# Performance work log

Measured on AMD Instinct MI355X. Metric: run time of the kernel, lower is better.

## Reference

```python
import jax, jax.numpy as jnp
import numpy as np
from jax import lax

B, EMB, CIN, COUT, K, H, W = 16, 768, 64, 64, 3, 112, 112
HID = EMB // 4  # reduction_ratio=4
TOTAL = COUT * CIN * K * K


def setup_inputs() -> dict:
    key = jax.random.key(0)
    k1, k2, k3, k4 = jax.random.split(key, 4)
    cls_token = jax.random.normal(k1, (B, 1, EMB), dtype=jnp.float32)
    features = jax.random.normal(k2, (B, CIN, H, W), dtype=jnp.float32)
    W1 = jax.random.normal(k3, (EMB, HID), dtype=jnp.float32) * 0.02
    b1 = jnp.zeros((HID,), dtype=jnp.float32)
    W2 = jax.random.normal(k4, (HID, TOTAL), dtype=jnp.float32) * 0.01
    b2 = jnp.zeros((TOTAL,), dtype=jnp.float32)
    return {"cls_token": cls_token, "features": features,
            "W1": W1, "b1": b1, "W2": W2, "b2": b2}


def _per_sample_conv(feat, kern):
    # feat: (CIN, H, W); kern: (COUT, CIN, K, K) -> (COUT, H, W)
    out = lax.conv_general_dilated(
        feat[None], kern, window_strides=(1, 1), padding="SAME",
        dimension_numbers=("NCHW", "OIHW", "NCHW"))
    return out[0]


def reference(cls_token, features, W1, b1, W2, b2):
    # Dynamic kernel generation from CLS token
    x = cls_token[:, 0, :]                      # (B, EMB)
    h = jax.nn.relu(x @ W1 + b1)                # (B, HID)
    params = jnp.tanh(h @ W2 + b2)              # (B, TOTAL)
    kernel = params.reshape(B, COUT, CIN, K, K)
    # Per-sample convolution (equivalent to unfold + bmm in torch)
    conv_feat = jax.vmap(_per_sample_conv)(features, kernel)  # (B, COUT, H, W)
    # in_channels == out_channels -> identity shortcut
    return conv_feat + features
```

## Files before the change

### kernel.cpp

```cpp
#include <hip/hip_runtime.h>
#include <hip/hip_bf16.h>

#define BB   16
#define EMB  768
#define CIN  64
#define COUT 64
#define HH   112
#define WW   112
#define HID  192
#define TOTAL 36864
#define KSZ  576
#define SCOLS 114
#define CELL  128
#define ROWB (SCOLS * CELL)

typedef short bf16x8 __attribute__((ext_vector_type(8)));
typedef float f32x4  __attribute__((ext_vector_type(4)));
typedef int   i32x4  __attribute__((ext_vector_type(4)));

static __device__ __forceinline__ unsigned short f2bf(float f) {
    unsigned u = __float_as_uint(f);
    u += 0x7FFF + ((u >> 16) & 1);
    return (unsigned short)(u >> 16);
}

static __device__ __forceinline__ bf16x8 pack8(const float* v) {
    bf16x8 r;
    #pragma unroll
    for (int j = 0; j < 8; ++j) r[j] = (short)f2bf(v[j]);
    return r;
}

__global__ __launch_bounds__(256) void mlp1_kernel(const float* __restrict__ cls,
                                                   const float* __restrict__ W1,
                                                   const float* __restrict__ b1,
                                                   float* __restrict__ h) {
    __shared__ float xs[EMB];
    __shared__ float red[16][17];
    const int b   = blockIdx.x / 12;
    const int jg  = blockIdx.x - 12 * b;
    const int tid = threadIdx.x;
    for (int i = tid; i < EMB; i += 256) xs[i] = cls[b * EMB + i];
    __syncthreads();
    const int j16 = tid & 15;
    const int kq  = tid >> 4;
    const int j   = jg * 16 + j16;
    float acc = 0.f;
    #pragma unroll
    for (int k = kq * 48; k < kq * 48 + 48; ++k) acc += xs[k] * W1[k * HID + j];
    red[j16][kq] = acc;
    __syncthreads();
    if (tid < 16) {
        float s = b1[jg * 16 + tid];
        #pragma unroll
        for (int q = 0; q < 16; ++q) s += red[tid][q];
        h[b * HID + jg * 16 + tid] = fmaxf(s, 0.f);
    }
}

__global__ __launch_bounds__(256) void mlp2_kernel(const float* __restrict__ h,
                                                   const float* __restrict__ W2,
                                                   const float* __restrict__ b2,
                                                   unsigned short* __restrict__ Ag) {
    __shared__ float hs[16 * 193];
    const int tid = threadIdx.x;
    for (int i = tid; i < BB * HID; i += 256) {
        const int bb = i / HID;
        hs[bb * 193 + (i - bb * HID)] = h[i];
    }
    __syncthreads();
    const int wave = tid >> 6;
    const int lane = tid & 63;
    const int lg   = lane >> 4;
    const int ln   = lane & 15;
    const int t0   = (blockIdx.x * 4 + wave) * 16;

    bf16x8 a6[6];
    #pragma unroll
    for (int kk = 0; kk < 6; ++kk) {
        float v[8];
        #pragma unroll
        for (int j = 0; j < 8; ++j) v[j] = hs[ln * 193 + kk * 32 + lg * 8 + j];
        a6[kk] = pack8(v);
    }

    f32x4 acc = (f32x4){0.f, 0.f, 0.f, 0.f};
    #pragma unroll
    for (int kk = 0; kk < 6; ++kk) {
        float w[8];
        #pragma unroll
        for (int j = 0; j < 8; ++j)
            w[j] = W2[(size_t)(kk * 32 + lg * 8 + j) * TOTAL + t0 + ln];
        acc = __builtin_amdgcn_mfma_f32_16x16x32_bf16(a6[kk], pack8(w), acc, 0, 0, 0);
    }

    const int t    = t0 + ln;
    const float bias = b2[t];
    const int co  = t / KSZ;
    const int rem = t - co * KSZ;
    const int ci  = rem / 9;
    const int p9  = rem - ci * 9;
    const float idv = (p9 == 4 && co == ci) ? 1.f : 0.f;
    unsigned short* pA = Ag + (size_t)(p9 * 64 + co) * 64 + ci;
    #pragma unroll
    for (int rg = 0; rg < 4; ++rg) {
        const int bi = lg * 4 + rg;
        pA[(size_t)bi * TOTAL] = f2bf(tanhf(acc[rg] + bias) + idv);
    }
}

__global__ __launch_bounds__(256) void conv_kernel(const float* __restrict__ feat,
                                                   const unsigned short* __restrict__ Ag,
                                                   float* __restrict__ out) {
    __shared__ __align__(16) char lds[4 * ROWB];
    const int tid = threadIdx.x;
    const int bid  = (blockIdx.x & 7) * 112 + (blockIdx.x >> 3);
    const int b    = bid / 56;
    const int tile = bid - b * 56;
    const int y0   = tile * 2;

    if (tid < 64) {
        const int zr = tid >> 4, zc = ((tid >> 3) & 1) ? (SCOLS - 1) : 0, zs = tid & 7;
        *(i32x4*)(lds + (zr * SCOLS + zc) * CELL + zs * 16) = (i32x4){0, 0, 0, 0};
    }

    {
        const int o  = tid >> 5;
        const int rr = (tid >> 3) & 3;
        const int xs = tid & 7;
        if (xs < 7) {
            const int y  = y0 - 1 + rr;
            const bool yv = (unsigned)y < HH;
            const float* fp = feat + (((size_t)b * CIN + o * 8) * HH + y) * WW + 4 * xs;
            const f32x4 z4 = {0.f, 0.f, 0.f, 0.f};
            char* ldsr = lds + rr * ROWB;
            #pragma unroll
            for (int sh = 0; sh < 2; ++sh) {
                f32x4 v[8][2];
                #pragma unroll
                for (int ss = 0; ss < 2; ++ss) {
                    const int s = sh * 2 + ss;
                    #pragma unroll
                    for (int j = 0; j < 8; ++j)
                        v[j][ss] = yv ? *(const f32x4*)(fp + (size_t)j * (HH * WW) + s * 28)
                                      : z4;
                }
                #pragma unroll
                for (int ss = 0; ss < 2; ++ss) {
                    const int s = sh * 2 + ss;
                    #pragma unroll
                    for (int j2 = 0; j2 < 4; ++j2) {
                        const int cell = 4 * (s * 7 + xs) + j2 + 1;
                        const int sl   = (o ^ (cell & 7) ^ rr) & 7;
                        const unsigned d0 = (unsigned)f2bf(v[0][ss][j2]) | ((unsigned)f2bf(v[1][ss][j2]) << 16);
                        const unsigned d1 = (unsigned)f2bf(v[2][ss][j2]) | ((unsigned)f2bf(v[3][ss][j2]) << 16);
                        const unsigned d2 = (unsigned)f2bf(v[4][ss][j2]) | ((unsigned)f2bf(v[5][ss][j2]) << 16);
                        const unsigned d3 = (unsigned)f2bf(v[6][ss][j2]) | ((unsigned)f2bf(v[7][ss][j2]) << 16);
                        *(i32x4*)(ldsr + cell * CELL + sl * 16) =
                            (i32x4){(int)d0, (int)d1, (int)d2, (int)d3};
                    }
                }
            }
        }
    }

    const int wave = tid >> 6;
    const int lane = tid & 63;
    const int cog  = wave & 1;
    const int r    = wave >> 1;
    const int lg   = lane >> 4;
    const int ln   = lane & 15;
    const unsigned short* Ab = Ag + (size_t)b * 9 * 4096;
    bf16x8 af[9][2][2];
    #pragma unroll
    for (int p9 = 0; p9 < 9; ++p9)
        #pragma unroll
        for (int ct = 0; ct < 2; ++ct)
            #pragma unroll
            for (int cib = 0; cib < 2; ++cib)
                af[p9][ct][cib] = *(const bf16x8*)(Ab + (size_t)(p9 * 64 + cog * 32 + ct * 16 + ln) * 64
                                                   + cib * 32 + lg * 8);
    __syncthreads();

    f32x4 acc[2][7];
    #pragma unroll
    for (int ct = 0; ct < 2; ++ct)
        #pragma unroll
        for (int t = 0; t < 7; ++t) acc[ct][t] = (f32x4){0.f, 0.f, 0.f, 0.f};

    #pragma unroll
    for (int p9 = 0; p9 < 9; ++p9) {
        const int kh = p9 / 3, kw = p9 - 3 * kh;
        const int rs = r + kh;
        const char* lbase = lds + rs * ROWB + (ln + kw) * CELL;
        const int   c7    = (ln + kw) & 7;
        #pragma unroll
        for (int cib = 0; cib < 2; ++cib) {
            const int sw = (((cib * 4 + lg) ^ c7 ^ rs) & 7) << 4;
            #pragma unroll
            for (int t = 0; t < 7; ++t) {
                const bf16x8 bf = *(const bf16x8*)(lbase + t * 2048 + sw);
                acc[0][t] = __builtin_amdgcn_mfma_f32_16x16x32_bf16(af[p9][0][cib], bf, acc[0][t], 0, 0, 0);
                acc[1][t] = __builtin_amdgcn_mfma_f32_16x16x32_bf16(af[p9][1][cib], bf, acc[1][t], 0, 0, 0);
            }
        }
    }

    const int y = y0 + r;
    float* ob = out + (((size_t)b * COUT + cog * 32 + lg * 4) * HH + y) * WW + ln;
    #pragma unroll
    for (int ct = 0; ct < 2; ++ct)
        #pragma unroll
        for (int t = 0; t < 7; ++t)
            #pragma unroll
            for (int rg = 0; rg < 4; ++rg)
                ob[((size_t)(ct * 16 + rg)) * HH * WW + t * 16] = acc[ct][t][rg];
}

extern "C" void kernel_launch(void* const* d_in, const int* in_sizes, int n_in,
                              void* d_out, int out_size, void* d_ws, size_t ws_size,
                              hipStream_t stream) {
    const float* cls      = (const float*)d_in[0];
    const float* features = (const float*)d_in[1];
    const float* W1       = (const float*)d_in[2];
    const float* b1       = (const float*)d_in[3];
    const float* W2       = (const float*)d_in[4];
    const float* b2       = (const float*)d_in[5];
    float* out = (float*)d_out;

    float*          h  = (float*)d_ws;
    unsigned short* Ag = (unsigned short*)(h + BB * HID);

    mlp1_kernel<<<192, 256, 0, stream>>>(cls, W1, b1, h);
    mlp2_kernel<<<TOTAL / 64, 256, 0, stream>>>(h, W2, b2, Ag);
    conv_kernel<<<56 * BB, 256, 0, stream>>>(feat\
ures, Ag, out);
}
```

Measured before the change: 58.32 us.

## Split conv input channels into two halves to halve LDS and weight registers

The conv kernel now stages input channels in two 32-channel halves, cutting the LDS tile from 4x114x128 to 4x114x64 bytes. Weight fragments are loaded per half and per tap inside the loop instead of being held in a large register array up front. Launch bounds now request 4 blocks per CU. The aim is higher occupancy through lower LDS and register use, at the cost of an extra barrier between halves and less overlap of the global loads with the MFMA work.

Measured after the change: 56.68 us. -2.8%, faster.

```diff
diff --git a/kernel.cpp b/kernel.cpp
--- a/kernel.cpp
+++ b/kernel.cpp
@@ -11,12 +11,13 @@
 #define TOTAL 36864
 #define KSZ  576
 #define SCOLS 114
-#define CELL  128
-#define ROWB (SCOLS * CELL)
+#define CELLH 64
+#define ROWBH (SCOLS * CELLH)
 
 typedef short bf16x8 __attribute__((ext_vector_type(8)));
 typedef float f32x4  __attribute__((ext_vector_type(4)));
 typedef int   i32x4  __attribute__((ext_vector_type(4)));
+typedef int   i32x2  __attribute__((ext_vector_type(2)));
 
 static __device__ __forceinline__ unsigned short f2bf(float f) {
     unsigned u = __float_as_uint(f);
@@ -109,60 +110,15 @@
     }
 }
 
-__global__ __launch_bounds__(256) void conv_kernel(const float* __restrict__ feat,
-                                                   const unsigned short* __restrict__ Ag,
-                                                   float* __restrict__ out) {
-    __shared__ __align__(16) char lds[4 * ROWB];
+__global__ __launch_bounds__(256, 4) void conv_kernel(const float* __restrict__ feat,
+                                                      const unsigned short* __restrict__ Ag,
+                                                      float* __restrict__ out) {
+    __shared__ __align__(16) char lds[4 * ROWBH];
     const int tid = threadIdx.x;
     const int bid  = (blockIdx.x & 7) * 112 + (blockIdx.x >> 3);
     const int b    = bid / 56;
     const int tile = bid - b * 56;
     const int y0   = tile * 2;
-
-    if (tid < 64) {
-        const int zr = tid >> 4, zc = ((tid >> 3) & 1) ? (SCOLS - 1) : 0, zs = tid & 7;
-        *(i32x4*)(lds + (zr * SCOLS + zc) * CELL + zs * 16) = (i32x4){0, 0, 0, 0};
-    }
-
-    {
-        const int o  = tid >> 5;
-        const int rr = (tid >> 3) & 3;
-        const int xs = tid & 7;
-        if (xs < 7) {
-            const int y  = y0 - 1 + rr;
-            const bool yv = (unsigned)y < HH;
-            const float* fp = feat + (((size_t)b * CIN + o * 8) * HH + y) * WW + 4 * xs;
-            const f32x4 z4 = {0.f, 0.f, 0.f, 0.f};
-            char* ldsr = lds + rr * ROWB;
-            #pragma unroll
-            for (int sh = 0; sh < 2; ++sh) {
-                f32x4 v[8][2];
-                #pragma unroll
-                for (int ss = 0; ss < 2; ++ss) {
-                    const int s = sh * 2 + ss;
-                    #pragma unroll
-                    for (int j = 0; j < 8; ++j)
-                        v[j][ss] = yv ? *(const f32x4*)(fp + (size_t)j * (HH * WW) + s * 28)
-                                      : z4;
-                }
-                #pragma unroll
-                for (int ss = 0; ss < 2; ++ss) {
-                    const int s = sh * 2 + ss;
-                    #pragma unroll
-                    for (int j2 = 0; j2 < 4; ++j2) {
-                        const int cell = 4 * (s * 7 + xs) + j2 + 1;
-                        const int sl   = (o ^ (cell & 7) ^ rr) & 7;
-                        const unsigned d0 = (unsigned)f2bf(v[0][ss][j2]) | ((unsigned)f2bf(v[1][ss][j2]) << 16);
-                        const unsigned d1 = (unsigned)f2bf(v[2][ss][j2]) | ((unsigned)f2bf(v[3][ss][j2]) << 16);
-                        const unsigned d2 = (unsigned)f2bf(v[4][ss][j2]) | ((unsigned)f2bf(v[5][ss][j2]) << 16);
-                        const unsigned d3 = (unsigned)f2bf(v[6][ss][j2]) | ((unsigned)f2bf(v[7][ss][j2]) << 16);
-                        *(i32x4*)(ldsr + cell * CELL + sl * 16) =
-                            (i32x4){(int)d0, (int)d1, (int)d2, (int)d3};
-                    }
-                }
-            }
-        }
-    }
 
     const int wave = tid >> 6;
     const int lane = tid & 63;
@@ -170,38 +126,72 @@
     const int r    = wave >> 1;
     const int lg   = lane >> 4;
     const int ln   = lane & 15;
+
+    const int so = tid >> 6;
+    const int sr = (tid >> 4) & 3;
+    const int sx = tid & 15;
+    const int sy = y0 - 1 + sr;
+    const bool sact = (sx < 14);
+    const bool syv  = sact && ((unsigned)sy < HH);
+    char* ldsr = lds + sr * ROWBH;
+    const f32x4 z4 = {0.f, 0.f, 0.f, 0.f};
+
+    f32x4 acc[2][7];
+    #pragma unroll
+    for (int ct = 0; ct < 2; ++ct)
+        #pragma unroll
+        for (int t = 0; t < 7; ++t) acc[ct][t] = (f32x4){0.f, 0.f, 0.f, 0.f};
+
     const unsigned short* Ab = Ag + (size_t)b * 9 * 4096;
-    bf16x8 af[9][2][2];
-    #pragma unroll
-    for (int p9 = 0; p9 < 9; ++p9)
-        #pragma unroll
-        for (int ct = 0; ct < 2; ++ct)
+
+    if (tid < 32) {
+        const int zr = tid >> 3, zc = ((tid >> 2) & 1) ? (SCOLS - 1) : 0, zs = tid & 3;
+        *(i32x4*)(lds + zr * ROWBH + zc * CELLH + zs * 16) = (i32x4){0, 0, 0, 0};
+    }
+
+    #pragma unroll
+    for (int h = 0; h < 2; ++h) {
+        if (h) __syncthreads();
+        if (sact) {
+            const float* fp = feat + (((size_t)b * CIN + h * 32 + so * 8) * HH + sy) * WW + 8 * sx;
             #pragma unroll
-            for (int cib = 0; cib < 2; ++cib)
-                af[p9][ct][cib] = *(const bf16x8*)(Ab + (size_t)(p9 * 64 + cog * 32 + ct * 16 + ln) * 64
-                                                   + cib * 32 + lg * 8);
-    __syncthreads();
-
-    f32x4 acc[2][7];
-    #pragma unroll
-    for (int ct = 0; ct < 2; ++ct)
-        #pragma unroll
-        for (int t = 0; t < 7; ++t) acc[ct][t] = (f32x4){0.f, 0.f, 0.f, 0.f};
-
-    #pragma unroll
-    for (int p9 = 0; p9 < 9; ++p9) {
-        const int kh = p9 / 3, kw = p9 - 3 * kh;
-        const int rs = r + kh;
-        const char* lbase = lds + rs * ROWB + (ln + kw) * CELL;
-        const int   c7    = (ln + kw) & 7;
-        #pragma unroll
-        for (int cib = 0; cib < 2; ++cib) {
-            const int sw = (((cib * 4 + lg) ^ c7 ^ rs) & 7) << 4;
+            for (int jb = 0; jb < 2; ++jb) {
+                f32x4 v[4][2];
+                #pragma unroll
+                for (int j = 0; j < 4; ++j)
+                    #pragma unroll
+                    for (int c = 0; c < 2; ++c)
+                        v[j][c] = syv ? *(const f32x4*)(fp + (size_t)(jb * 4 + j) * (HH * WW) + 4 * c)
+                                      : z4;
+                #pragma unroll
+                for (int i = 0; i < 8; ++i) {
+                    const int cell = 8 * sx + i + 1;
+                    const int sl   = (so ^ (cell & 3) ^ sr) & 3;
+                    const int c = i >> 2, e = i & 3;
+                    const unsigned d0 = (unsigned)f2bf(v[0][c][e]) | ((unsigned)f2bf(v[1][c][e]) << 16);
+                    const unsigned d1 = (unsigned)f2bf(v[2][c][e]) | ((unsigned)f2bf(v[3][c][e]) << 16);
+                    *(i32x2*)(ldsr + cell * CELLH + sl * 16 + jb * 8) = (i32x2){(int)d0, (int)d1};
+                }
+            }
+        }
+        __syncthreads();
+
+        #pragma unroll
+        for (int p9 = 0; p9 < 9; ++p9) {
+            const int kh = p9 / 3, kw = p9 - 3 * kh;
+            const int rs = r + kh;
+            const bf16x8 a0 = *(const bf16x8*)(Ab + (size_t)(p9 * 64 + cog * 32 + ln) * 64
+                                               + h * 32 + lg * 8);
+            const bf16x8 a1 = *(const bf16x8*)(Ab + (size_t)(p9 * 64 + cog * 32 + 16 + ln) * 64
+                                               + h * 32 + lg * 8);
+            const char* lbase = lds + rs * ROWBH;
             #pragma unroll
             for (int t = 0; t < 7; ++t) {
-                const bf16x8 bf = *(const bf16x8*)(lbase + t * 2048 + sw);
-                acc[0][t] = __builtin_amdgcn_mfma_f32_16x16x32_bf16(af[p9][0][cib], bf, acc[0][t], 0, 0, 0);
-                acc[1][t] = __builtin_amdgcn_mfma_f32_16x16x32_bf16(af[p9][1][cib], bf, acc[1][t], 0, 0, 0);
+                const int cell = ln + kw + 16 * t;
+                const int sl   = (lg ^ (cell & 3) ^ rs) & 3;
+                const bf16x8 bf = *(const bf16x8*)(lbase + cell * CELLH + sl * 16);
+                acc[0][t] = __builtin_amdgcn_mfma_f32_16x16x32_bf16(a0, bf, acc[0][t], 0, 0, 0);
+                acc[1][t] = __builtin_amdgcn_mfma_f32_16x16x32_bf16(a1, bf, acc[1][t], 0, 0, 0);
             }
         }
     }
@@ -233,6 +223,5 @@
 
     mlp1_kernel<<<192, 256, 0, stream>>>(cls, W1, b1, h);
     mlp2_kernel<<<TOTAL / 64, 256, 0, stream>>>(h, W2, b2, Ag);
-    conv_kernel<<<56 * BB, 256, 0, stream>>>(feat\
-ures, Ag, out);
-}
+    conv_kernel<<<56 * BB, 256, 0, stream>>>(features, Ag, out);
+}
```

## Pre-pack padded bf16 feature plane and stream into LDS via global_load_lds

Applied to the files above, without the earlier changes.

Adds a pre-pass, fused with the first MLP kernel, that converts features to a zero-padded channel-last bf16 buffer in workspace. The conv kernel then fills LDS directly with async global_load_lds copies that apply the XOR swizzle, replacing its per-block fp32 load, convert and LDS store. Each input row was previously converted once per overlapping tile, and the halo rows twice, so this removes redundant conversion and halves the bytes the conv kernel reads. The cost is an extra write and read of the bf16 buffer through global memory. It also relies on workspace being large enough for the padded plane.

Measured after the change: 60.58 us. 1.04x slower.

```diff
diff --git a/kernel.cpp b/kernel.cpp
--- a/kernel.cpp
+++ b/kernel.cpp
@@ -10,9 +10,9 @@
 #define HID  192
 #define TOTAL 36864
 #define KSZ  576
-#define SCOLS 114
-#define CELL  128
-#define ROWB (SCOLS * CELL)
+#define PW   114
+#define CELL 128
+#define ROWB (PW * CELL)
 
 typedef short bf16x8 __attribute__((ext_vector_type(8)));
 typedef float f32x4  __attribute__((ext_vector_type(4)));
@@ -31,30 +31,74 @@
     return r;
 }
 
-__global__ __launch_bounds__(256) void mlp1_kernel(const float* __restrict__ cls,
-                                                   const float* __restrict__ W1,
-                                                   const float* __restrict__ b1,
-                                                   float* __restrict__ h) {
-    __shared__ float xs[EMB];
-    __shared__ float red[16][17];
-    const int b   = blockIdx.x / 12;
-    const int jg  = blockIdx.x - 12 * b;
+#define GLOAD_LDS16(g, l) \
+    __builtin_amdgcn_global_load_lds((const __attribute__((address_space(1))) void*)(g), \
+                                     (__attribute__((address_space(3))) void*)(l), 16, 0, 0)
+
+__global__ __launch_bounds__(256) void pre_mlp1(const float* __restrict__ feat,
+                                                unsigned short* __restrict__ P,
+                                                const float* __restrict__ cls,
+                                                const float* __restrict__ W1,
+                                                const float* __restrict__ b1,
+                                                float* __restrict__ h) {
+    __shared__ float smem[EMB + 16 * 17];
+    const int bid = blockIdx.x;
     const int tid = threadIdx.x;
-    for (int i = tid; i < EMB; i += 256) xs[i] = cls[b * EMB + i];
-    __syncthreads();
-    const int j16 = tid & 15;
-    const int kq  = tid >> 4;
-    const int j   = jg * 16 + j16;
-    float acc = 0.f;
-    #pragma unroll
-    for (int k = kq * 48; k < kq * 48 + 48; ++k) acc += xs[k] * W1[k * HID + j];
-    red[j16][kq] = acc;
-    __syncthreads();
-    if (tid < 16) {
-        float s = b1[jg * 16 + tid];
-        #pragma unroll
-        for (int q = 0; q < 16; ++q) s += red[tid][q];
-        h[b * HID + jg * 16 + tid] = fmaxf(s, 0.f);
+
+    if (bid < HH * BB) {
+        const int b = bid & 15;
+        const int y = bid >> 4;
+        unsigned short* Prow = P + ((size_t)b * PW + y + 1) * (PW * 64);
+        if (tid < 16) {
+            const int cell = (tid >> 3) ? (PW - 1) : 0;
+            *(i32x4*)((char*)Prow + cell * CELL + (tid & 7) * 16) = (i32x4){0, 0, 0, 0};
+        }
+        const int o = tid >> 5;
+        const int q = tid & 31;
+        if (q < 28) {
+            const float* fb = feat + (((size_t)b * CIN + o * 8) * HH + y) * WW + 4 * q;
+            f32x4 v[8];
+            #pragma unroll
+            for (int j = 0; j < 8; ++j) v[j] = *(const f32x4*)(fb + (size_t)j * (HH * WW));
+            #pragma unroll
+            for (int i = 0; i < 4; ++i) {
+                unsigned short w[8];
+                #pragma unroll
+                for (int j = 0; j < 8; ++j) w[j] = f2bf(v[j][i]);
+                *(bf16x8*)(Prow + (size_t)(4 * q + i + 1) * 64 + o * 8) = *(bf16x8*)w;
+            }
+        }
+    } else if (bid < HH * BB + 32) {
+        const int idx = bid - HH * BB;
+        const int b = idx & 15;
+        unsigned short* Prow = P + ((size_t)b * PW + ((idx >> 4) ? (PW - 1) : 0)) * (PW * 64);
+        #pragma unroll
+        for (int k = 0; k < 4; ++k) {
+            const int i = tid + 256 * k;
+            if (i < 912) ((i32x4*)Prow)[i] = (i32x4){0, 0, 0, 0};
+        }
+    } else {
+        float* xs  = smem;
+        float* red = smem + EMB;
+        const int idx = bid - (HH * BB + 32);
+        const int b   = idx / 12;
+        const int jg  = idx - 12 * b;
+        for (int i = tid; i < EMB; i += 256) xs[i] = cls[b * EMB + i];
+        __syncthreads();
+        const int j16 = tid & 15;
+        const int kq  = tid >> 4;
+        const int j   = jg * 16 + j16;
+        float acc = 0.f;
+        #pragma unroll
+        for (int k = kq * 48; k < kq * 48 + 48; ++k) acc += xs[k] * W1[k * HID + j];
+        red[j16 * 17 + kq] = acc;
+        __syncthreads();
+        if (tid < 16) {
+            float s = b1[jg * 16 + tid];
+            #pragma unroll
+            for (int q = 0; q < 16; ++q) s += red[tid * 17 + q];
+            h[b * HID + jg * 16 + tid] = fmaxf(s, 0.f);
+        }
     }
 }
 
@@ -109,8 +153,8 @@
     }
 }
 
-__global__ __launch_bounds__(256) void conv_kernel(const float* __restrict__ feat,
-                                                   const unsigned short* __restrict__ Ag,
+__global__ __launch_bounds__(256) void conv_kernel(const unsigned short* __restrict__ Ag,
+                                                   const unsigned short* __restrict__ P,
                                                    float* __restrict__ out) {
     __shared__ __align__(16) char lds[4 * ROWB];
     const int tid = threadIdx.x;
@@ -119,49 +163,22 @@
     const int tile = bid - b * 56;
     const int y0   = tile * 2;
 
+    const char* Prow0 = (const char*)(P + ((size_t)b * PW + y0) * (PW * 64));
+    #pragma unroll
+    for (int it = 0; it < 14; ++it) {
+        const int i = it * 256 + tid;
+        const int s = i / 912;
+        const int j = i - s * 912;
+        const int c = j >> 3, g = j & 7;
+        GLOAD_LDS16(Prow0 + (size_t)s * ROWB + c * CELL + ((g ^ (c & 7)) << 4),
+                    lds + (size_t)i * 16);
+    }
     if (tid < 64) {
-        const int zr = tid >> 4, zc = ((tid >> 3) & 1) ? (SCOLS - 1) : 0, zs = tid & 7;
-        *(i32x4*)(lds + (zr * SCOLS + zc) * CELL + zs * 16) = (i32x4){0, 0, 0, 0};
-    }
-
-    {
-        const int o  = tid >> 5;
-        const int rr = (tid >> 3) & 3;
-        const int xs = tid & 7;
-        if (xs < 7) {
-            const int y  = y0 - 1 + rr;
-            const bool yv = (unsigned)y < HH;
-            const float* fp = feat + (((size_t)b * CIN + o * 8) * HH + y) * WW + 4 * xs;
-            const f32x4 z4 = {0.f, 0.f, 0.f, 0.f};
-            char* ldsr = lds + rr * ROWB;
-            #pragma unroll
-            for (int sh = 0; sh < 2; ++sh) {
-                f32x4 v[8][2];
-                #pragma unroll
-                for (int ss = 0; ss < 2; ++ss) {
-                    const int s = sh * 2 + ss;
-                    #pragma unroll
-                    for (int j = 0; j < 8; ++j)
-                        v[j][ss] = yv ? *(const f32x4*)(fp + (size_t)j * (HH * WW) + s * 28)
-                                      : z4;
-                }
-                #pragma unroll
-                for (int ss = 0; ss < 2; ++ss) {
-                    const int s = sh * 2 + ss;
-                    #pragma unroll
-                    for (int j2 = 0; j2 < 4; ++j2) {
-                        const int cell = 4 * (s * 7 + xs) + j2 + 1;
-                        const int sl   = (o ^ (cell & 7) ^ rr) & 7;
-                        const unsigned d0 = (unsigned)f2bf(v[0][ss][j2]) | ((unsigned)f2bf(v[1][ss][j2]) << 16);
-                        const unsigned d1 = (unsigned)f2bf(v[2][ss][j2]) | ((unsigned)f2bf(v[3][ss][j2]) << 16);
-                        const unsigned d2 = (unsigned)f2bf(v[4][ss][j2]) | ((unsigned)f2bf(v[5][ss][j2]) << 16);
-                        const unsigned d3 = (unsigned)f2bf(v[6][ss][j2]) | ((unsigned)f2bf(v[7][ss][j2]) << 16);
-                        *(i32x4*)(ldsr + cell * CELL + sl * 16) =
-                            (i32x4){(int)d0, (int)d1, (int)d2, (int)d3};
-                    }
-                }
-            }
-        }
+        const int i = 3584 + tid;
+        const int j = i - 3 * 912;
+        const int c = j >> 3, g = j & 7;
+        GLOAD_LDS16(Prow0 + (size_t)3 * ROWB + c * CELL + ((g ^ (c & 7)) << 4),
+                    lds + (size_t)i * 16);
     }
 
     const int wave = tid >> 6;
@@ -191,12 +208,11 @@
     #pragma unroll
     for (int p9 = 0; p9 < 9; ++p9) {
         const int kh = p9 / 3, kw = p9 - 3 * kh;
-        const int rs = r + kh;
-        const char* lbase = lds + rs * ROWB + (ln + kw) * CELL;
+        const char* lbase = lds + (r + kh) * ROWB + (ln + kw) * CELL;
         const int   c7    = (ln + kw) & 7;
         #pragma unroll
         for (int cib = 0; cib < 2; ++cib) {
-            const int sw = (((cib * 4 + lg) ^ c7 ^ rs) & 7) << 4;
+            const int sw = ((cib * 4 + lg) ^ c7) << 4;
             #pragma unroll
             for (int t = 0; t < 7; ++t) {
                 const bf16x8 bf = *(const bf16x8*)(lbase + t * 2048 + sw);
@@ -230,9 +246,9 @@
 
     float*          h  = (float*)d_ws;
     unsigned short* Ag = (unsigned short*)(h + BB * HID);
-
-    mlp1_kernel<<<192, 256, 0, stream>>>(cls, W1, b1, h);
+    unsigned short* P  = Ag + (size_t)BB * 9 * 4096;
+
+    pre_mlp1<<<HH * BB + 32 + 192, 256, 0, stream>>>(features, P, cls, W1, b1, h);
     mlp2_kernel<<<TOTAL / 64, 256, 0, stream>>>(h, W2, b2, Ag);
-    conv_kernel<<<56 * BB, 256, 0, stream>>>(feat\
-ures, Ag, out);
-}
+    conv_kernel<<<56 * BB, 256, 0, stream>>>(Ag, P, out);
+}
```
